# Kernel optimization log

Measured on AMD Instinct MI355X. Metric: run time of the kernel, lower is better.

## Reference

```python
import jax, jax.numpy as jnp
import numpy as np

WH, WW = 7, 7          # window_size
DIM = 384
NH = 12
HD = DIM // NH
CS = 2                 # channel_scale
SCALE = HD ** -0.5
BWIN = 2048            # num_windows * batch
N = WH * WW            # kv tokens per window = 49
QN = (2 * WH) * (2 * WW)  # query tokens = 196


def _relative_position_index():
    # mirrors the torch buffer construction exactly (numpy, static)
    ch = np.repeat(np.arange(WH), 2)
    cw = np.repeat(np.arange(WW), 2)
    gh, gw = np.meshgrid(ch, cw, indexing='ij')          # (2Wh, 2Ww)
    flat = np.stack([gh.reshape(-1), gw.reshape(-1)])    # (2, 4N)
    rel = flat[:, :, None] - flat[:, None, :]            # (2, 4N, 4N)
    rel = rel[:, :, ::4]                                 # (2, 4N, N)
    rel = np.transpose(rel, (1, 2, 0)).copy()            # (4N, N, 2)
    rel[:, :, 0] += WH - 1
    rel[:, :, 1] += WW - 1
    rel[:, :, 0] *= 2 * WW - 1
    return rel.sum(-1)                                   # (4N, N) int

REL_IDX = jnp.asarray(_relative_position_index())


def setup_inputs() -> dict:
    key = jax.random.key(0)
    ks = jax.random.split(key, 9)
    tbl_rows = (2 * 2 * WH - 1) * (2 * 2 * WW - 1)       # 729
    return {
        'kv': jax.random.normal(ks[0], (BWIN, N, DIM), jnp.float32),
        'q': jax.random.normal(ks[1], (BWIN, QN, DIM // CS), jnp.float32),
        'w_kv': jax.random.normal(ks[2], (DIM, 2 * DIM), jnp.float32) * 0.02,
        'b_kv': jax.random.normal(ks[3], (2 * DIM,), jnp.float32) * 0.02,
        'w_q': jax.random.normal(ks[4], (DIM // CS, DIM), jnp.float32) * 0.02,
        'b_q': jax.random.normal(ks[5], (DIM,), jnp.float32) * 0.02,
        'bias_table': jax.random.normal(ks[6], (tbl_rows, NH), jnp.float32) * 0.02,
        'w_proj': jax.random.normal(ks[7], (DIM, DIM // CS), jnp.float32) * 0.02,
        'b_proj': jax.random.normal(ks[8], (DIM // CS,), jnp.float32) * 0.02,
    }


def reference(kv, q, w_kv, b_kv, w_q, b_q, bias_table, w_proj, b_proj):
    B, Nk, C = kv.shape
    Qn = q.shape[1]
    # projections
    kvp = kv @ w_kv + b_kv                               # (B, N, 2C)
    kvp = kvp.reshape(B, Nk, 2, NH, HD)
    k = kvp[:, :, 0]                                     # (B, N, H, hd)
    v = kvp[:, :, 1]
    qp = (q @ w_q + b_q).reshape(B, Qn, NH, HD)
    # windowed cross attention with gathered relative position bias
    attn = jnp.einsum('bqhd,bkhd->bhqk', qp * SCALE, k)  # (B, H, 4N, N)
    bias = bias_table[REL_IDX]                           # (4N, N, H)
    attn = attn + jnp.transpose(bias, (2, 0, 1))[None]
    attn = jax.nn.softmax(attn, axis=-1)
    out = jnp.einsum('bhqk,bkhd->bqhd', attn, v).reshape(B, Qn, C)
    return out @ w_proj + b_proj                          # (B, 4N, C//2)
```

## Files before the change

### kernel.cpp

```cpp
#include <hip/hip_runtime.h>

#define BWIN 2048
#define NKV  49
#define DIM  384
#define NH   12
#define HD   32
#define QN   196
#define KQ   192
#define SCALE 0.17677669529663687f

#define KS_STR  392
#define VT_STR  72
#define QT_STR  200
#define OB_STR  40
#define QP_STR  40
#define P_STR   72

#define OFF_KS   0
#define OFF_VT   (NKV * KS_STR)
#define OFF_BIAS (OFF_VT + NH * HD * VT_STR)
#define OFF_UC   (OFF_BIAS + 169 * NH)
#define OFF_QT   OFF_UC
#define OFF_OB   (OFF_QT + 16 * QT_STR)
#define OFF_QP   (OFF_OB + NH * 16 * OB_STR)
#define OFF_P    (OFF_QP + NH * 16 * QP_STR)
#define LDS_TOT  (OFF_P + NH * 16 * P_STR)

typedef __bf16 bf16x8 __attribute__((ext_vector_type(8)));
typedef float  f32x4  __attribute__((ext_vector_type(4)));
typedef unsigned short u16;
typedef unsigned int   u32;

__device__ __forceinline__ int imin(int a, int b) { return a < b ? a : b; }

__device__ __forceinline__ u16 f2b(float f) {
    u32 u = __builtin_bit_cast(u32, f);
    return (u16)((u + 0x7fffu + ((u >> 16) & 1u)) >> 16);
}
__device__ __forceinline__ float b2f(u16 h) {
    return __builtin_bit_cast(float, ((u32)h) << 16);
}
__device__ __forceinline__ bf16x8 ld_frag(const u16* p) {
    uint4 v = *(const uint4*)p;
    return __builtin_bit_cast(bf16x8, v);
}
__device__ __forceinline__ void lds_fence() {
    asm volatile("s_waitcnt lgkmcnt(0)" ::: "memory");
}
#define MFMA(a, b, c) __builtin_amdgcn_mfma_f32_16x16x32_bf16((a), (b), (c), 0, 0, 0)

__global__ void prep_weights(const float* __restrict__ w_kv, const float* __restrict__ w_q,
                             const float* __restrict__ w_proj, u16* __restrict__ wbuf) {
    int i = blockIdx.x * 512 + threadIdx.x;
    if (i < 294912) {
        int n = i / 384, k = i % 384;
        wbuf[i] = f2b(w_kv[k * 768 + n]);
    } else if (i < 368640) {
        int j = i - 294912;
        int n = j / 192, k = j % 192;
        wbuf[i] = f2b(w_q[k * 384 + n]);
    } else {
        int j = i - 368640;
        int n = j / 384, k = j % 384;
        wbuf[i] = f2b(w_proj[k * 192 + n]);
    }
}

__global__ __launch_bounds__(768, 3) void wca_fused(
    const float* __restrict__ kv, const float* __restrict__ q,
    const float* __restrict__ b_kv, const float* __restrict__ b_q,
    const float* __restrict__ bias_table, const float* __restrict__ b_proj,
    const u16* __restrict__ wkvT, const u16* __restrict__ wqT, const u16* __restrict__ wprojT,
    float* __restrict__ out) {

    __shared__ u16 lds[LDS_TOT];

    const int tid  = threadIdx.x;
    const int b    = blockIdx.x;
    const int wave = tid >> 6, lane = tid & 63, ln = lane & 15, quad = lane >> 4;
    const int h    = wave;

    u16* ks     = lds + OFF_KS;
    u16* vt     = lds + OFF_VT;
    u16* bias_s = lds + OFF_BIAS;
    u16* kvs    = lds + OFF_UC;
    u16* qtile  = lds + OFF_QT;
    u16* obuf   = lds + OFF_OB;
    u16* qp_s   = lds + OFF_QP + h * (16 * QP_STR);
    u16* P_s    = lds + OFF_P  + h * (16 * P_STR);

    {
        const float4* src = (const float4*)(kv + (size_t)b * NKV * DIM);
        for (int c = tid; c < NKV * DIM / 4; c += 768) {
            int r = c / (DIM / 4), c4 = c % (DIM / 4);
            float4 f = src[c];
            ushort4 u; u.x = f2b(f.x); u.y = f2b(f.y); u.z = f2b(f.z); u.w = f2b(f.w);
            *(ushort4*)&kvs[r * KS_STR + c4 * 4] = u;
        }
        for (int c = tid; c < 169 * NH; c += 768) bias_s[c] = f2b(bias_table[c]);
        for (int c = tid; c < NH * HD * VT_STR; c += 768) vt[c] = 0;
    }
    __syncthreads();

    {
        const int cb = h * HD;
        f32x4 acc[4][4];
#pragma unroll
        for (int j = 0; j < 4; j++)
#pragma unroll
            for (int m = 0; m < 4; m++) acc[j][m] = (f32x4){0.f, 0.f, 0.f, 0.f};
        const u16* wb[4] = {
            wkvT + (size_t)(cb + ln) * DIM,
            wkvT + (size_t)(cb + 16 + ln) * DIM,
            wkvT + (size_t)(DIM + cb + ln) * DIM,
            wkvT + (size_t)(DIM + cb + 16 + ln) * DIM };
        const u16* ar[4] = {
            &kvs[imin(ln,      NKV - 1) * KS_STR],
            &kvs[imin(16 + ln, NKV - 1) * KS_STR],
            &kvs[imin(32 + ln, NKV - 1) * KS_STR],
            &kvs[imin(48 + ln, NKV - 1) * KS_STR] };
#pragma unroll
        for (int k = 0; k < 12; k++) {
            bf16x8 b0 = ld_frag(wb[0] + k * 32 + quad * 8);
            bf16x8 b1 = ld_frag(wb[1] + k * 32 + quad * 8);
            bf16x8 b2 = ld_frag(wb[2] + k * 32 + quad * 8);
            bf16x8 b3 = ld_frag(wb[3] + k * 32 + quad * 8);
#pragma unroll
            for (int m = 0; m < 4; m++) {
                bf16x8 a = ld_frag(ar[m] + k * 32 + quad * 8);
                acc[0][m] = MFMA(a, b0, acc[0][m]);
                acc[1][m] = MFMA(a, b1, acc[1][m]);
                acc[2][m] = MFMA(a, b2, acc[2][m]);
                acc[3][m] = MFMA(a, b3, acc[3][m]);
            }
        }
        float bk0 = b_kv[cb + ln],       bk1 = b_kv[cb + 16 + ln];
        float bv0 = b_kv[DIM + cb + ln], bv1 = b_kv[DIM + cb + 16 + ln];
        u16* vth = vt + h * (HD * VT_STR);
#pragma unroll
        for (int m = 0; m < 4; m++)
#pragma unroll
            for (int r = 0; r < 4; r++) {
                int kk = m * 16 + quad * 4 + r;
                if (kk < NKV) {
                    ks[kk * KS_STR + cb + ln]      = f2b(acc[0][m][r] + bk0);
                    ks[kk * KS_STR + cb + 16 + ln] = f2b(acc[1][m][r] + bk1);
                    vth[ln * VT_STR + kk]          = f2b(acc[2][m][r] + bv0);
                    vth[(16 + ln) * VT_STR + kk]   = f2b(acc[3][m][r] + bv1);
                }
            }
    }
    __syncthreads();

    int  kterm[4];  bool kval[4];
#pragma unroll
    for (int n = 0; n < 4; n++) {
        int kk = n * 16 + ln;
        int t4 = 4 * kk, kA = t4 / 14, kB = t4 - kA * 14;
        kterm[n] = 84 - 13 * (kA >> 1) - (kB >> 1);
        kval[n]  = (kk < NKV);
    }
    const float bq0 = b_q[h * HD + ln], bq1 = b_q[h * HD + 16 + ln];
    const float bpj = b_proj[h * 16 + ln];
    const f32x4 z4 = {0.f, 0.f, 0.f, 0.f};

    bf16x8 wqf[2][6];
#pragma unroll
    for (int k = 0; k < 6; k++) {
        wqf[0][k] = ld_frag(&wqT[(size_t)(h * HD + ln) * KQ + k * 32 + quad * 8]);
        wqf[1][k] = ld_frag(&wqT[(size_t)(h * HD + 16 + ln) * KQ + k * 32 + quad * 8]);
    }

    {
        int rr = tid / 48, c4 = tid % 48;
        int qrow = imin(rr, QN - 1);
        float4 f = *(const float4*)(q + ((size_t)b * QN + qrow) * KQ + c4 * 4);
        ushort4 u; u.x = f2b(f.x); u.y = f2b(f.y); u.z = f2b(f.z); u.w = f2b(f.w);
        *(ushort4*)&qtile[rr * QT_STR + c4 * 4] = u;
    }
    __syncthreads();

    for (int t = 0; t < 13; ++t) {
        f32x4 qa0 = z4, qa1 = z4;
        {
            const u16* qrp = &qtile[ln * QT_STR + quad * 8];
#pragma unroll
            for (int k = 0; k < 6; k++) {
                bf16x8 a = ld_frag(qrp + k * 32);
                qa0 = MFMA(a, wqf[0][k], qa0);
                qa1 = MFMA(a, wqf[1][k], qa1);
            }
        }
#pragma unroll
        for (int r = 0; r < 4; r++) {
            qp_s[(quad * 4 + r) * QP_STR + ln]      = f2b((qa0[r] + bq0) * SCALE);
            qp_s[(quad * 4 + r) * QP_STR + 16 + ln] = f2b((qa1[r] + bq1) * SCALE);
        }
        lds_fence();

        bf16x8 aq = ld_frag(&qp_s[ln * QP_STR + quad * 8]);
        f32x4 s[4];
#pragma unroll
        for (int n = 0; n < 4; n++) {
            bf16x8 bk = ld_frag(&ks[imin(n * 16 + ln, NKV - 1) * KS_STR + h * HD + quad * 8]);
            s[n] = MFMA(aq, bk, z4);
        }
        float rsum[4];
#pragma unroll
        for (int r = 0; r < 4; r++) {
            int qrow = t * 16 + quad * 4 + r;
            int qb = imin(qrow, QN - 1);
            int aqd = qb / 14, bqd = qb - aqd * 14;
            int qterm = 13 * (aqd >> 1) + (bqd >> 1);
            float sv[4];
#pragma unroll
            for (int n = 0; n < 4; n++) {
                if (kval[n]) sv[n] = s[n][r] + b2f(bias_s[(qterm + kterm[n]) * NH + h]);
                else         sv[n] = -1e30f;
            }
            float mx = fmaxf(fmaxf(sv[0], sv[1]), fmaxf(sv[2], sv[3]));
            mx = fmaxf(mx, __shfl_xor(mx, 1));
            mx = fmaxf(mx, __shfl_xor(mx, 2));
            mx = fmaxf(mx, __shfl_xor(mx, 4));
            mx = fmaxf(mx, __shfl_xor(mx, 8));
            float e[4], sum = 0.f;
#pragma unroll
            for (int n = 0; n < 4; n++) { e[n] = __expf(sv[n] - mx); sum += e[n]; }
            sum += __shfl_xor(sum, 1);
            sum += __shfl_xor(sum, 2);
            sum += __shfl_xor(sum, 4);
            sum += __shfl_xor(sum, 8);
            rsum[r] = sum;
#pragma unroll
            for (int n = 0; n < 4; n++)
                P_s[(quad * 4 + r) * P_STR + n * 16 + ln] = f2b(e[n]);
        }
        lds_fence();

        {
            bf16x8 ap0 = ld_frag(&P_s[ln * P_STR + quad * 8]);
            bf16x8 ap1 = ld_frag(&P_s[ln * P_STR + 32 + quad * 8]);
            const u16* vth = &vt[h * (HD * VT_STR)];
            bf16x8 bv00 = ld_frag(&vth[ln * VT_STR + quad * 8]);
            bf16x8 bv01 = ld_frag(&vth[ln * VT_STR + 32 + quad * 8]);
            bf16x8 bv10 = ld_frag(&vth[(16 + ln) * VT_STR + quad * 8]);
            bf16x8 bv11 = ld_frag(&vth[(16 + ln) * VT_STR + 32 + quad * 8]);
            f32x4 o0 = MFMA(ap0, bv00, z4); o0 = MFMA(ap1, bv01, o0);
            f32x4 o1 = MFMA(ap0, bv10, z4); o1 = MFMA(ap1, bv11, o1);
#pragma unroll
            for (int r = 0; r < 4; r++) {
                float rinv = 1.0f / rsum[r];
                obuf[h * 640 + (quad * 4 + r) * OB_STR + ln]      = f2b(o0[r] * rinv);
                obuf[h * 640 + (quad * 4 + r) * OB_STR + 16 + ln] = f2b(o1[r] * rinv);
            }
        }
        __syncthreads();

        if (t < 12) {
            int rr = tid / 48, c4 = tid % 48;
            int qrow = imin((t + 1) * 16 + rr, QN - 1);
            float4 f = *(const float4*)(q + ((size_t)b * QN + qrow) * KQ + c4 * 4);
            ushort4 u; u.x = f2b(f.x); u.y = f2b(f.y); u.z = f2b(f.z); u.w = f2b(f.w);
            *(ushort4*)&qtile[rr * QT_STR + c4 * 4] = u;
        }

        {
            f32x4 p0 = z4, p1 = z4;
#pragma unroll
            for (int hh = 0; hh < NH; hh += 2) {
                p0 = MFMA(ld_frag(&obuf[hh * 640 + ln * OB_STR + quad * 8]),
                          ld_frag(&wprojT[(size_t)(h * 16 + ln) * DIM + hh * HD + quad * 8]), p0);
                p1 = MFMA(ld_frag(&obuf[(hh + 1) * 640 + ln * OB_STR + quad * 8]),
                          ld_frag(&wprojT[(size_t)(h * 16 + ln) * DIM + (hh + 1) * HD + quad * 8]), p1);
            }
#pragma unroll
            for (int r = 0; r < 4; r++) {
                int qrow = t * 16 + quad * 4 + r;
                if (qrow < QN)
                    out[((size_t)b * QN + qrow) * KQ + h * 16 + ln] = p0[r] + p1[r] + bpj;
            }
        }
        __syncthreads();
    }
}

extern "C" void kernel_launch(void* const* d_in, const int* in_sizes, int n_in,
                              void* d_out, int out_size, void* d_ws, size_t ws_size,
                              hipStream_t stream) {
    (void)in_sizes; (void)n_in; (void)out_size; (void)ws_size;
    const float* kv         = (const float*)d_in[0];
    const float* q          = (const float*)d_in[1];
    const float* w_kv       = (const float*)d_in[2];
    const float* b_kv       = (const float*)d_in[3];
    const float* w_q        = (const float*)d_in[4];
    const float* b_q        = (const float*)d_in[5];
    const float* bias_table = (const float*)d_in[6];
    const float* w_proj     = (const float*)d_in[7];
    const float* b_proj     = (const float*)d_in[8];
    float* out = (float*)d_out;
    u16* wbuf = (u16*)d_ws;

    prep_weights<<<864, 512, 0, stream>>>(w_kv, w_q, w_proj, wbuf);
    wca_fused<<<BWIN, 768, 0, stream>>>(kv, q, b_kv, b_q, bias_table, b_proj,
                                        wbuf, wbuf + 294912, wbuf + 368640, out);
}
```

Measured before the change: 1.732 ms.

## Shrink LDS footprint by holding K/V fragments in registers, reuse union buffer

The per-window K and V^T tiles are no longer kept in LDS. Each wave stages its head's K/V through a scratch area in two rounds, then holds the MFMA B-fragments in registers for the whole query loop. LDS use drops from about 80KB to about 68KB and the launch bound asks for 6 waves per SIMD instead of 3, aiming for more concurrent blocks. The Q scale is folded into the weights, Wq fragments are reloaded from global each tile instead of held in registers, and the next Q tile is prefetched into registers early. The risks are more register pressure, extra barriers during staging, and more repeated global or L2 weight loads.

```diff
diff --git a/kernel.cpp b/kernel.cpp
--- a/kernel.cpp
+++ b/kernel.cpp
@@ -9,22 +9,21 @@
 #define KQ   192
 #define SCALE 0.17677669529663687f
 
-#define KS_STR  392
-#define VT_STR  72
+#define OFF_U   2032
+#define UNI_SZ  32384
+#define LDS_TOT (OFF_U + UNI_SZ)
+
+#define KV_STR  392
 #define QT_STR  200
 #define OB_STR  40
 #define QP_STR  40
 #define P_STR   72
-
-#define OFF_KS   0
-#define OFF_VT   (NKV * KS_STR)
-#define OFF_BIAS (OFF_VT + NH * HD * VT_STR)
-#define OFF_UC   (OFF_BIAS + 169 * NH)
-#define OFF_QT   OFF_UC
-#define OFF_OB   (OFF_QT + 16 * QT_STR)
-#define OFF_QP   (OFF_OB + NH * 16 * OB_STR)
-#define OFF_P    (OFF_QP + NH * 16 * QP_STR)
-#define LDS_TOT  (OFF_P + NH * 16 * P_STR)
+#define SCK_STR 40
+#define SCV_STR 72
+#define U_QT    0
+#define U_OB    3200
+#define U_QP    10880
+#define U_P     18560
 
 typedef __bf16 bf16x8 __attribute__((ext_vector_type(8)));
 typedef float  f32x4  __attribute__((ext_vector_type(4)));
@@ -58,7 +57,7 @@
     } else if (i < 368640) {
         int j = i - 294912;
         int n = j / 192, k = j % 192;
-        wbuf[i] = f2b(w_q[k * 384 + n]);
+        wbuf[i] = f2b(w_q[k * 384 + n] * SCALE);
     } else {
         int j = i - 368640;
         int n = j / 384, k = j % 384;
@@ -66,7 +65,7 @@
     }
 }
 
-__global__ __launch_bounds__(768, 3) void wca_fused(
+__global__ __launch_bounds__(768, 6) void wca_fused(
     const float* __restrict__ kv, const float* __restrict__ q,
     const float* __restrict__ b_kv, const float* __restrict__ b_q,
     const float* __restrict__ bias_table, const float* __restrict__ b_proj,
@@ -79,15 +78,15 @@
     const int b    = blockIdx.x;
     const int wave = tid >> 6, lane = tid & 63, ln = lane & 15, quad = lane >> 4;
     const int h    = wave;
-
-    u16* ks     = lds + OFF_KS;
-    u16* vt     = lds + OFF_VT;
-    u16* bias_s = lds + OFF_BIAS;
-    u16* kvs    = lds + OFF_UC;
-    u16* qtile  = lds + OFF_QT;
-    u16* obuf   = lds + OFF_OB;
-    u16* qp_s   = lds + OFF_QP + h * (16 * QP_STR);
-    u16* P_s    = lds + OFF_P  + h * (16 * P_STR);
+    const int cb   = h * HD;
+
+    u16* bias_s = lds;
+    u16* uni    = lds + OFF_U;
+    u16* kvs    = uni;
+    u16* qtile  = uni + U_QT;
+    u16* obuf   = uni + U_OB;
+    u16* qp_s   = uni + U_QP + h * (16 * QP_STR);
+    u16* P_s    = uni + U_P  + h * (16 * P_STR);
 
     {
         const float4* src = (const float4*)(kv + (size_t)b * NKV * DIM);
@@ -95,116 +94,126 @@
             int r = c / (DIM / 4), c4 = c % (DIM / 4);
             float4 f = src[c];
             ushort4 u; u.x = f2b(f.x); u.y = f2b(f.y); u.z = f2b(f.z); u.w = f2b(f.w);
-            *(ushort4*)&kvs[r * KS_STR + c4 * 4] = u;
+            *(ushort4*)&kvs[r * KV_STR + c4 * 4] = u;
         }
         for (int c = tid; c < 169 * NH; c += 768) bias_s[c] = f2b(bias_table[c]);
-        for (int c = tid; c < NH * HD * VT_STR; c += 768) vt[c] = 0;
     }
     __syncthreads();
 
+    f32x4 acc[4][4];
+#pragma unroll
+    for (int j = 0; j < 4; j++)
+#pragma unroll
+        for (int m = 0; m < 4; m++) acc[j][m] = (f32x4){0.f, 0.f, 0.f, 0.f};
     {
-        const int cb = h * HD;
-        f32x4 acc[4][4];
-#pragma unroll
-        for (int j = 0; j < 4; j++)
-#pragma unroll
-            for (int m = 0; m < 4; m++) acc[j][m] = (f32x4){0.f, 0.f, 0.f, 0.f};
-        const u16* wb[4] = {
-            wkvT + (size_t)(cb + ln) * DIM,
-            wkvT + (size_t)(cb + 16 + ln) * DIM,
-            wkvT + (size_t)(DIM + cb + ln) * DIM,
-            wkvT + (size_t)(DIM + cb + 16 + ln) * DIM };
         const u16* ar[4] = {
-            &kvs[imin(ln,      NKV - 1) * KS_STR],
-            &kvs[imin(16 + ln, NKV - 1) * KS_STR],
-            &kvs[imin(32 + ln, NKV - 1) * KS_STR],
-            &kvs[imin(48 + ln, NKV - 1) * KS_STR] };
-#pragma unroll
-        for (int k = 0; k < 12; k++) {
-            bf16x8 b0 = ld_frag(wb[0] + k * 32 + quad * 8);
-            bf16x8 b1 = ld_frag(wb[1] + k * 32 + quad * 8);
-            bf16x8 b2 = ld_frag(wb[2] + k * 32 + quad * 8);
-            bf16x8 b3 = ld_frag(wb[3] + k * 32 + quad * 8);
-#pragma unroll
-            for (int m = 0; m < 4; m++) {
-                bf16x8 a = ld_frag(ar[m] + k * 32 + quad * 8);
-                acc[0][m] = MFMA(a, b0, acc[0][m]);
-                acc[1][m] = MFMA(a, b1, acc[1][m]);
-                acc[2][m] = MFMA(a, b2, acc[2][m]);
-                acc[3][m] = MFMA(a, b3, acc[3][m]);
-            }
-        }
-        float bk0 = b_kv[cb + ln],       bk1 = b_kv[cb + 16 + ln];
-        float bv0 = b_kv[DIM + cb + ln], bv1 = b_kv[DIM + cb + 16 + ln];
-        u16* vth = vt + h * (HD * VT_STR);
-#pragma unroll
-        for (int m = 0; m < 4; m++)
-#pragma unroll
-            for (int r = 0; r < 4; r++) {
-                int kk = m * 16 + quad * 4 + r;
-                if (kk < NKV) {
-                    ks[kk * KS_STR + cb + ln]      = f2b(acc[0][m][r] + bk0);
-                    ks[kk * KS_STR + cb + 16 + ln] = f2b(acc[1][m][r] + bk1);
-                    vth[ln * VT_STR + kk]          = f2b(acc[2][m][r] + bv0);
-                    vth[(16 + ln) * VT_STR + kk]   = f2b(acc[3][m][r] + bv1);
+            &kvs[imin(ln,      NKV - 1) * KV_STR + quad * 8],
+            &kvs[imin(16 + ln, NKV - 1) * KV_STR + quad * 8],
+            &kvs[imin(32 + ln, NKV - 1) * KV_STR + quad * 8],
+            &kvs[imin(48 + ln, NKV - 1) * KV_STR + quad * 8] };
+#pragma unroll 1
+        for (int half = 0; half < 2; ++half) {
+            const u16* w0 = wkvT + (size_t)(half * DIM + cb + ln) * DIM + quad * 8;
+            const u16* w1 = wkvT + (size_t)(half * DIM + cb + 16 + ln) * DIM + quad * 8;
+#pragma unroll
+            for (int k = 0; k < 12; k++) {
+                bf16x8 b0 = ld_frag(w0 + k * 32);
+                bf16x8 b1 = ld_frag(w1 + k * 32);
+#pragma unroll
+                for (int m = 0; m < 4; m++) {
+                    bf16x8 a = ld_frag(ar[m] + k * 32);
+                    acc[half * 2 + 0][m] = MFMA(a, b0, acc[half * 2 + 0][m]);
+                    acc[half * 2 + 1][m] = MFMA(a, b1, acc[half * 2 + 1][m]);
                 }
             }
+        }
     }
     __syncthreads();
 
-    int  kterm[4];  bool kval[4];
+    bf16x8 bk[4];
+    bf16x8 bvf[4];
+    {
+        const float bk0 = b_kv[cb + ln],       bk1 = b_kv[cb + 16 + ln];
+        const float bv0 = b_kv[DIM + cb + ln], bv1 = b_kv[DIM + cb + 16 + ln];
+#pragma unroll 1
+        for (int rnd = 0; rnd < 2; ++rnd) {
+            if (wave / 6 == rnd) {
+                u16* scK = uni + (wave - rnd * 6) * (1960 + 2304);
+                u16* scV = scK + 1960;
+                for (int i = lane; i < HD * SCV_STR; i += 64) scV[i] = 0;
+#pragma unroll
+                for (int m = 0; m < 4; m++)
+#pragma unroll
+                    for (int r = 0; r < 4; r++) {
+                        int kk = m * 16 + quad * 4 + r;
+                        if (kk < NKV) {
+                            scK[kk * SCK_STR + ln]        = f2b(acc[0][m][r] + bk0);
+                            scK[kk * SCK_STR + 16 + ln]   = f2b(acc[1][m][r] + bk1);
+                            scV[ln * SCV_STR + kk]        = f2b(acc[2][m][r] + bv0);
+                            scV[(16 + ln) * SCV_STR + kk] = f2b(acc[3][m][r] + bv1);
+                        }
+                    }
+                lds_fence();
+#pragma unroll
+                for (int n = 0; n < 4; n++)
+                    bk[n] = ld_frag(&scK[imin(n * 16 + ln, NKV - 1) * SCK_STR + quad * 8]);
+#pragma unroll
+                for (int dt = 0; dt < 2; dt++)
+#pragma unroll
+                    for (int kt = 0; kt < 2; kt++)
+                        bvf[dt * 2 + kt] = ld_frag(&scV[(dt * 16 + ln) * SCV_STR + kt * 32 + quad * 8]);
+            }
+            __syncthreads();
+        }
+    }
+
+    int kterm[4];
 #pragma unroll
     for (int n = 0; n < 4; n++) {
         int kk = n * 16 + ln;
         int t4 = 4 * kk, kA = t4 / 14, kB = t4 - kA * 14;
         kterm[n] = 84 - 13 * (kA >> 1) - (kB >> 1);
-        kval[n]  = (kk < NKV);
-    }
-    const float bq0 = b_q[h * HD + ln], bq1 = b_q[h * HD + 16 + ln];
+    }
+    const bool k3ok = (ln == 0);
+    const float bq0 = b_q[cb + ln] * SCALE, bq1 = b_q[cb + 16 + ln] * SCALE;
     const float bpj = b_proj[h * 16 + ln];
     const f32x4 z4 = {0.f, 0.f, 0.f, 0.f};
-
-    bf16x8 wqf[2][6];
-#pragma unroll
-    for (int k = 0; k < 6; k++) {
-        wqf[0][k] = ld_frag(&wqT[(size_t)(h * HD + ln) * KQ + k * 32 + quad * 8]);
-        wqf[1][k] = ld_frag(&wqT[(size_t)(h * HD + 16 + ln) * KQ + k * 32 + quad * 8]);
-    }
+    const u16* wq0 = wqT + (size_t)(cb + ln) * KQ + quad * 8;
+    const u16* wq1 = wqT + (size_t)(cb + 16 + ln) * KQ + quad * 8;
+    const u16* wpr = wprojT + (size_t)(h * 16 + ln) * DIM + quad * 8;
+    const int  rr = tid / 48, c4 = tid % 48;
+    const float* qbase = q + (size_t)b * QN * KQ + c4 * 4;
 
     {
-        int rr = tid / 48, c4 = tid % 48;
-        int qrow = imin(rr, QN - 1);
-        float4 f = *(const float4*)(q + ((size_t)b * QN + qrow) * KQ + c4 * 4);
+        float4 f = *(const float4*)(qbase + (size_t)imin(rr, QN - 1) * KQ);
         ushort4 u; u.x = f2b(f.x); u.y = f2b(f.y); u.z = f2b(f.z); u.w = f2b(f.w);
         *(ushort4*)&qtile[rr * QT_STR + c4 * 4] = u;
     }
     __syncthreads();
 
     for (int t = 0; t < 13; ++t) {
+        float4 qn;
+        if (t < 12) qn = *(const float4*)(qbase + (size_t)imin((t + 1) * 16 + rr, QN - 1) * KQ);
+
         f32x4 qa0 = z4, qa1 = z4;
-        {
-            const u16* qrp = &qtile[ln * QT_STR + quad * 8];
-#pragma unroll
-            for (int k = 0; k < 6; k++) {
-                bf16x8 a = ld_frag(qrp + k * 32);
-                qa0 = MFMA(a, wqf[0][k], qa0);
-                qa1 = MFMA(a, wqf[1][k], qa1);
-            }
+#pragma unroll
+        for (int k = 0; k < 6; k++) {
+            bf16x8 a = ld_frag(&qtile[ln * QT_STR + k * 32 + quad * 8]);
+            qa0 = MFMA(a, ld_frag(wq0 + k * 32), qa0);
+            qa1 = MFMA(a, ld_frag(wq1 + k * 32), qa1);
         }
 #pragma unroll
         for (int r = 0; r < 4; r++) {
-            qp_s[(quad * 4 + r) * QP_STR + ln]      = f2b((qa0[r] + bq0) * SCALE);
-            qp_s[(quad * 4 + r) * QP_STR + 16 + ln] = f2b((qa1[r] + bq1) * SCALE);
+            qp_s[(quad * 4 + r) * QP_STR + ln]      = f2b(qa0[r] + bq0);
+            qp_s[(quad * 4 + r) * QP_STR + 16 + ln] = f2b(qa1[r] + bq1);
         }
         lds_fence();
 
         bf16x8 aq = ld_frag(&qp_s[ln * QP_STR + quad * 8]);
         f32x4 s[4];
 #pragma unroll
-        for (int n = 0; n < 4; n++) {
-            bf16x8 bk = ld_frag(&ks[imin(n * 16 + ln, NKV - 1) * KS_STR + h * HD + quad * 8]);
-            s[n] = MFMA(aq, bk, z4);
-        }
+        for (int n = 0; n < 4; n++) s[n] = MFMA(aq, bk[n], z4);
+
         float rsum[4];
 #pragma unroll
         for (int r = 0; r < 4; r++) {
@@ -214,10 +223,9 @@
             int qterm = 13 * (aqd >> 1) + (bqd >> 1);
             float sv[4];
 #pragma unroll
-            for (int n = 0; n < 4; n++) {
-                if (kval[n]) sv[n] = s[n][r] + b2f(bias_s[(qterm + kterm[n]) * NH + h]);
-                else         sv[n] = -1e30f;
-            }
+            for (int n = 0; n < 3; n++) sv[n] = s[n][r] + b2f(bias_s[(qterm + kterm[n]) * NH + h]);
+            sv[3] = -1e30f;
+            if (k3ok) sv[3] = s[3][r] + b2f(bias_s[(qterm + kterm[3]) * NH + h]);
             float mx = fmaxf(fmaxf(sv[0], sv[1]), fmaxf(sv[2], sv[3]));
             mx = fmaxf(mx, __shfl_xor(mx, 1));
             mx = fmaxf(mx, __shfl_xor(mx, 2));
@@ -240,13 +248,8 @@
         {
             bf16x8 ap0 = ld_frag(&P_s[ln * P_STR + quad * 8]);
             bf16x8 ap1 = ld_frag(&P_s[ln * P_STR + 32 + quad * 8]);
-            const u16* vth = &vt[h * (HD * VT_STR)];
-            bf16x8 bv00 = ld_frag(&vth[ln * VT_STR + quad * 8]);
-            bf16x8 bv01 = ld_frag(&vth[ln * VT_STR + 32 + quad * 8]);
-            bf16x8 bv10 = ld_frag(&vth[(16 + ln) * VT_STR + quad * 8]);
-            bf16x8 bv11 = ld_frag(&vth[(16 + ln) * VT_STR + 32 + quad * 8]);
-            f32x4 o0 = MFMA(ap0, bv00, z4); o0 = MFMA(ap1, bv01, o0);
-            f32x4 o1 = MFMA(ap0, bv10, z4); o1 = MFMA(ap1, bv11, o1);
+            f32x4 o0 = MFMA(ap0, bvf[0], z4); o0 = MFMA(ap1, bvf[1], o0);
+            f32x4 o1 = MFMA(ap0, bvf[2], z4); o1 = MFMA(ap1, bvf[3], o1);
 #pragma unroll
             for (int r = 0; r < 4; r++) {
                 float rinv = 1.0f / rsum[r];
@@ -257,10 +260,7 @@
         __syncthreads();
 
         if (t < 12) {
-            int rr = tid / 48, c4 = tid % 48;
-            int qrow = imin((t + 1) * 16 + rr, QN - 1);
-            float4 f = *(const float4*)(q + ((size_t)b * QN + qrow) * KQ + c4 * 4);
-            ushort4 u; u.x = f2b(f.x); u.y = f2b(f.y); u.z = f2b(f.z); u.w = f2b(f.w);
+            ushort4 u; u.x = f2b(qn.x); u.y = f2b(qn.y); u.z = f2b(qn.z); u.w = f2b(qn.w);
             *(ushort4*)&qtile[rr * QT_STR + c4 * 4] = u;
         }
 
@@ -269,9 +269,9 @@
 #pragma unroll
             for (int hh = 0; hh < NH; hh += 2) {
                 p0 = MFMA(ld_frag(&obuf[hh * 640 + ln * OB_STR + quad * 8]),
-                          ld_frag(&wprojT[(size_t)(h * 16 + ln) * DIM + hh * HD + quad * 8]), p0);
+                          ld_frag(wpr + hh * 32), p0);
                 p1 = MFMA(ld_frag(&obuf[(hh + 1) * 640 + ln * OB_STR + quad * 8]),
-                          ld_frag(&wprojT[(size_t)(h * 16 + ln) * DIM + (hh + 1) * HD + quad * 8]), p1);
+                          ld_frag(wpr + (hh + 1) * 32), p1);
             }
 #pragma unroll
             for (int r = 0; r < 4; r++) {
```

After: 2.697 ms. 55.7% more time.
